# Kernel tuning notes

Hardware: AMD Instinct MI355X
Metric: run time of the kernel (lower is better)

Reference implementation:

```python
import jax, jax.numpy as jnp
import numpy as np
from jax import lax

PH = PW = 7  # patch size


def _unfold2d(x, ph, pw):
    # x: [B, C, H, W] -> patches [B*Ho*Wo, C*ph*pw], channel-major like F.unfold
    B, C, H, W = x.shape
    patches = lax.conv_general_dilated_patches(
        x, filter_shape=(ph, pw), window_strides=(1, 1), padding='VALID')
    # patches: [B, C*ph*pw, Ho, Wo] with feature order (c, i, j) matching F.unfold
    Ho, Wo = H - ph + 1, W - pw + 1
    D = C * ph * pw
    q2d = patches.reshape(B, D, Ho * Wo).transpose(0, 2, 1).reshape(B * Ho * Wo, D)
    return q2d, (B, C, H, W, Ho, Wo, D)


def _fold2d_mean(res, shape_info):
    # res: [B*Ho*Wo, D] patch values -> overlap-add mean image [B, C, H, W]
    B, C, H, W, Ho, Wo, D = shape_info
    res = res.reshape(B, Ho, Wo, C, PH, PW)
    out = jnp.zeros((B, C, H, W), dtype=res.dtype)
    cnt = jnp.zeros((H, W), dtype=res.dtype)
    for di in range(PH):          # small fixed 7x7 loop over patch offsets
        for dj in range(PW):
            out = out.at[:, :, di:di + Ho, dj:dj + Wo].add(
                res[:, :, :, :, di, dj].transpose(0, 3, 1, 2))
            cnt = cnt.at[di:di + Ho, dj:dj + Wo].add(1.0)
    return out / cnt  # reduce='mean'


def setup_inputs() -> dict:
    key = jax.random.key(0)
    k1, k2, k3 = jax.random.split(key, 3)
    query = jax.random.normal(k1, (1, 3, 96, 96), dtype=jnp.float32)
    kmat = jax.random.normal(k2, (8100, 147), dtype=jnp.float32)
    vmat = jax.random.normal(k3, (8100, 147), dtype=jnp.float32)
    return {"query": query, "key": kmat, "value": vmat}


def reference(query, key, value):
    # 1) unfold query image into patch rows [Nq, D]
    q2d, shape_info = _unfold2d(query, PH, PW)
    # 2) nearest-neighbor lookup: squared-euclidean argmin over key rows
    qn = jnp.sum(q2d * q2d, axis=1, keepdims=True)        # [Nq, 1]
    kn = jnp.sum(key * key, axis=1)                       # [Nk]
    dist = qn + kn[None, :] - 2.0 * (q2d @ key.T)         # [Nq, Nk]
    idx = jnp.argmin(dist, axis=1)                        # [Nq]
    # 3) gather matched value patches and fold back (overlap-add mean)
    res = value[idx]                                      # [Nq, D]
    return _fold2d_mean(res, shape_info)
```

## Files before the change

### kernel.cpp

```cpp
#include <hip/hip_runtime.h>


#define NQ 8100
#define NK 8100
#define DD 147
#define HO 90
#define IMG 96
#define NCH 5
#define CST 262144
#define ARRN (NCH * CST)

typedef _Float16 half8 __attribute__((ext_vector_type(8)));
typedef float f32x4 __attribute__((ext_vector_type(4)));

__global__ void k_prep(const float* __restrict__ query, const float* __restrict__ key,
                       _Float16* __restrict__ Qh, _Float16* __restrict__ Ql,
                       _Float16* __restrict__ Kh, _Float16* __restrict__ Kl,
                       float* __restrict__ kn, unsigned long long* __restrict__ fidx64) {
    const int bx = blockIdx.x;
    const bool isK = (blockIdx.y != 0);

    if (bx >= 640) {
        if (!isK) return;
        int wave = threadIdx.x >> 6, lane = threadIdx.x & 63;
        int kb = ((bx - 640) * 4 + wave) * 16;
        for (int r = 0; r < 16; ++r) {
            int k = kb + r;
            float s = 0.f;
            if (k < NK)
                for (int d = lane; d < DD; d += 64) {
                    float v = key[k * DD + d];
                    s += v * v;
                }
#pragma unroll
            for (int off = 32; off; off >>= 1) s += __shfl_down(s, off, 64);
            if (lane == 0) {
                kn[k] = (k < NK) ? s : 1e30f;
                fidx64[k] = 0xFFFFFFFFFFFFFFFFull;
            }
        }
        return;
    }

    int t = bx * 256 + threadIdx.x;
    int c = t >> 15;
    int rem = t & 32767;
    int col = ((rem >> 6) << 4) + (rem & 15);
    int quad = (rem >> 4) & 3;
    int kbase = c * 32 + quad * 8;

    float v[8];
#pragma unroll
    for (int j = 0; j < 8; ++j) {
        int k = kbase + j;
        float x = 0.f;
        if (k < DD && col < NQ) {
            if (isK) {
                x = key[col * DD + k];
            } else {
                int c3 = k / 49, r2 = k - 49 * c3;
                int rr = r2 / 7, ss = r2 - 7 * rr;
                int y = col / HO, xx = col - HO * y;
                x = query[(c3 * IMG + y + rr) * IMG + xx + ss];
            }
        }
        v[j] = x;
    }
    half8 h8, l8;
#pragma unroll
    for (int j = 0; j < 8; ++j) {
        _Float16 h = (_Float16)v[j];
        h8[j] = h;
        l8[j] = (_Float16)((v[j] - (float)h) * 2048.0f);
    }
    if (isK) {
        *(half8*)(Kh + t * 8) = h8;
        *(half8*)(Kl + t * 8) = l8;
    } else {
        *(half8*)(Qh + t * 8) = h8;
        *(half8*)(Ql + t * 8) = l8;
    }
}

__launch_bounds__(256, 2)
__global__ void k_nn(const _Float16* __restrict__ Qh, const _Float16* __restrict__ Ql,
                     const _Float16* __restrict__ Kh, const _Float16* __restrict__ Kl,
                     const float* __restrict__ kn, unsigned long long* __restrict__ out) {
    __shared__ __align__(16) char smem[33792];

    const int tid = (int)threadIdx.x;
    const int wave = tid >> 6, lane = tid & 63;
    const int l15 = lane & 15, quad = lane >> 4;

    const int b = (int)blockIdx.x;
    const int xcd = b & 7;
    const int i = b >> 3;
    const int qt = (xcd >> 1) * 16 + (i & 15);
    const int kt = (xcd & 1) * 32 + (i >> 4);

    const int mbase = (wave >> 1) * 64;
    const int nbase = (wave & 1) * 64;
    const int q0 = qt * 128, n0 = kt * 128;

    const int agrp = (mbase >> 4);
    const int bgrp = (nbase >> 4);
    const _Float16* gQh = Qh + (qt * 8 + agrp) * 512 + lane * 8;
    const _Float16* gQl = Ql + (qt * 8 + agrp) * 512 + lane * 8;
    const _Float16* gKh = Kh + (kt * 8 + bgrp) * 512 + lane * 8;
    const _Float16* gKl = Kl + (kt * 8 + bgrp) * 512 + lane * 8;

    f32x4 acc0[4][4], acc1[4][4];
#pragma unroll
    for (int ii = 0; ii < 4; ++ii)
#pragma unroll
        for (int j = 0; j < 4; ++j) {
            acc0[ii][j] = (f32x4)0.f;
            acc1[ii][j] = (f32x4)0.f;
        }

#pragma unroll
    for (int c = 0; c < NCH; ++c) {
        half8 ah[4], al[4], bh[4], bl[4];
#pragma unroll
        for (int mt = 0; mt < 4; ++mt) {
            ah[mt] = *(const half8*)(gQh + c * CST + mt * 512);
            al[mt] = *(const half8*)(gQl + c * CST + mt * 512);
        }
#pragma unroll
        for (int nt = 0; nt < 4; ++nt) {
            bh[nt] = *(const half8*)(gKh + c * CST + nt * 512);
            bl[nt] = *(const half8*)(gKl + c * CST + nt * 512);
        }

        __builtin_amdgcn_s_setprio(1);
#pragma unroll
        for (int nt = 0; nt < 4; ++nt) {
#pragma unroll
            for (int mt = 0; mt < 4; ++mt) {
                acc0[mt][nt] = __builtin_amdgcn_mfma_f32_16x16x32_f16(ah[mt], bh[nt], acc0[mt][nt], 0, 0, 0);
                acc1[mt][nt] = __builtin_amdgcn_mfma_f32_16x16x32_f16(ah[mt], bl[nt], acc1[mt][nt], 0, 0, 0);
                acc1[mt][nt] = __builtin_amdgcn_mfma_f32_16x16x32_f16(al[mt], bh[nt], acc1[mt][nt], 0, 0, 0);
            }
        }
        __builtin_amdgcn_s_setprio(0);
    }

    float knv[4];
    int nglob[4];
#pragma unroll
    for (int nt = 0; nt < 4; ++nt) {
        nglob[nt] = n0 + nbase + nt * 16 + l15;
        knv[nt] = kn[nglob[nt]];
    }
    unsigned long long* redu = (unsigned long long*)smem;

#pragma unroll
    for (int mt = 0; mt < 4; ++mt)
#pragma unroll
        for (int r = 0; r < 4; ++r) {
            float bv = 1e38f;
            int bn = 0x7fffffff;
#pragma unroll
            for (int nt = 0; nt < 4; ++nt) {
                float d = knv[nt] - 2.0f * (acc0[mt][nt][r] + acc1[mt][nt][r] * (1.0f / 2048.0f));
                if (d < bv) { bv = d; bn = nglob[nt]; }
            }
            int m = mbase + mt * 16 + quad * 4 + r;
            int cidx = (nbase >> 2) + l15;
            unsigned u = __float_as_uint(bv);
            u = (u & 0x80000000u) ? ~u : (u | 0x80000000u);
            redu[m * 33 + cidx] = ((unsigned long long)u << 32) | (unsigned)bn;
        }
    __syncthreads();

    {
        int row = tid >> 1;
        int base = (tid & 1) * 16;
        unsigned long long best = 0xFFFFFFFFFFFFFFFFull;
        const unsigned long long* rp = redu + row * 33 + base;
#pragma unroll
        for (int t2 = 0; t2 < 16; ++t2) {
            unsigned long long v = rp[t2];
            best = (v < best) ? v : best;
        }
        unsigned long long other = __shfl_xor(best, 1, 64);
        best = (other < best) ? other : best;
        if (!(tid & 1)) atomicMin(&out[q0 + row], best);
    }
}

__global__ void k_fold(const float* __restrict__ value,
                       const unsigned long long* __restrict__ fidx64,
                       float* __restrict__ out) {
    int t = blockIdx.x * 256 + threadIdx.x;
    int pix = t >> 3, s = t & 7;
    if (pix >= 3 * IMG * IMG) return;
    int c = pix / (IMG * IMG);
    int rem = pix % (IMG * IMG);
    int Y = rem / IMG, X = rem % IMG;

    float partial = 0.f;
    int yy = Y - s;
    if (s < 7 && (unsigned)yy < (unsigned)HO) {
        const unsigned* fidx32 = (const unsigned*)fidx64;
        const float* vbase = value + c * 49 + s * 7;
        int rows[7];
        bool oks[7];
#pragma unroll
        for (int j = 0; j < 7; ++j) {
            int xx = X - j;
            bool ok = (unsigned)xx < (unsigned)HO;
            int p = ok ? (yy * HO + xx) : 0;
            rows[j] = (int)fidx32[2 * p];
            oks[j] = ok;
        }
#pragma unroll
        for (int j = 0; j < 7; ++j) {
            float v = vbase[rows[j] * DD + j];
            if (oks[j]) partial += v;
        }
    }
    partial += __shfl_down(partial, 4, 8);
    partial += __shfl_down(partial, 2, 8);
    partial += __shfl_down(partial, 1, 8);
    if (s == 0) {
        int i0 = max(0, Y - (HO - 1)), i1 = min(6, Y);
        int j0 = max(0, X - (HO - 1)), j1 = min(6, X);
        float cnt = (float)((i1 - i0 + 1) * (j1 - j0 + 1));
        out[pix] = partial / cnt;
    }
}

extern "C" void kernel_launch(void* const* d_in, const int* in_sizes, int n_in,
                              void* d_out, int out_size, void* d_ws, size_t ws_size,
                              hipStream_t stream) {
    const float* query = (const float*)d_in[0];
    const float* key   = (const float*)d_in[1];
    const float* value = (const float*)d_in[2];
    float* out = (float*)d_out;

    _Float16* Qh = (_Float16*)d_ws;
    _Float16* Ql = Qh + ARRN;
    _Float16* Kh = Ql + ARRN;
    _Float16* Kl = Kh + ARRN;
    float* kn = (float*)(Kl + ARRN);
    unsigned long long* fidx64 = (unsigned long long*)(kn + 8192);

    dim3 gp(768, 2);
    k_prep<<<gp, 256, 0, stream>>>(query, key, Qh, Ql, Kh, Kl, kn, fidx64);
    k_nn<<<4096, 256, 0, stream>>>(Qh, Ql, Kh, Kl, kn, fidx64);
    k_fold<<<864, 256, 0, stream>>>(value, fidx64, out);
}
```

Baseline: 144.2 us.

## Merge split-fp16 accumulators and double-buffer chunk fragment loads in NN kernel

The low half of each split-fp16 value is now stored unscaled, so all three MFMA products go into one accumulator instead of two. This halves accumulator registers and removes the rescale in the epilogue. Fragment loads for the next K chunk are also issued before the current chunk's MFMAs to hide global-load latency. The risk is that unscaled low residuals can underflow into fp16 subnormals, losing precision and possibly changing argmin ties; the register saving is partly spent on the doubled fragment buffers.

Result: no change. 145.3 us (+0.7%).

```diff
diff --git a/kernel.cpp b/kernel.cpp
--- a/kernel.cpp
+++ b/kernel.cpp
@@ -71,7 +71,7 @@
     for (int j = 0; j < 8; ++j) {
         _Float16 h = (_Float16)v[j];
         h8[j] = h;
-        l8[j] = (_Float16)((v[j] - (float)h) * 2048.0f);
+        l8[j] = (_Float16)(v[j] - (float)h);
     }
     if (isK) {
         *(half8*)(Kh + t * 8) = h8;
@@ -109,37 +109,49 @@
     const _Float16* gKh = Kh + (kt * 8 + bgrp) * 512 + lane * 8;
     const _Float16* gKl = Kl + (kt * 8 + bgrp) * 512 + lane * 8;
 
-    f32x4 acc0[4][4], acc1[4][4];
+    f32x4 acc[4][4];
 #pragma unroll
     for (int ii = 0; ii < 4; ++ii)
 #pragma unroll
-        for (int j = 0; j < 4; ++j) {
-            acc0[ii][j] = (f32x4)0.f;
-            acc1[ii][j] = (f32x4)0.f;
-        }
+        for (int j = 0; j < 4; ++j)
+            acc[ii][j] = (f32x4)0.f;
+
+    half8 ah[2][4], al[2][4], bh[2][4], bl[2][4];
+#pragma unroll
+    for (int mt = 0; mt < 4; ++mt) {
+        ah[0][mt] = *(const half8*)(gQh + mt * 512);
+        al[0][mt] = *(const half8*)(gQl + mt * 512);
+    }
+#pragma unroll
+    for (int nt = 0; nt < 4; ++nt) {
+        bh[0][nt] = *(const half8*)(gKh + nt * 512);
+        bl[0][nt] = *(const half8*)(gKl + nt * 512);
+    }
 
 #pragma unroll
     for (int c = 0; c < NCH; ++c) {
-        half8 ah[4], al[4], bh[4], bl[4];
-#pragma unroll
-        for (int mt = 0; mt < 4; ++mt) {
-            ah[mt] = *(const half8*)(gQh + c * CST + mt * 512);
-            al[mt] = *(const half8*)(gQl + c * CST + mt * 512);
-        }
+        const int cur = c & 1, nxt = cur ^ 1;
+        if (c + 1 < NCH) {
+#pragma unroll
+            for (int mt = 0; mt < 4; ++mt) {
+                ah[nxt][mt] = *(const half8*)(gQh + (c + 1) * CST + mt * 512);
+                al[nxt][mt] = *(const half8*)(gQl + (c + 1) * CST + mt * 512);
+            }
+#pragma unroll
+            for (int nt = 0; nt < 4; ++nt) {
+                bh[nxt][nt] = *(const half8*)(gKh + (c + 1) * CST + nt * 512);
+                bl[nxt][nt] = *(const half8*)(gKl + (c + 1) * CST + nt * 512);
+            }
+        }
+
+        __builtin_amdgcn_s_setprio(1);
 #pragma unroll
         for (int nt = 0; nt < 4; ++nt) {
-            bh[nt] = *(const half8*)(gKh + c * CST + nt * 512);
-            bl[nt] = *(const half8*)(gKl + c * CST + nt * 512);
-        }
-
-        __builtin_amdgcn_s_setprio(1);
-#pragma unroll
-        for (int nt = 0; nt < 4; ++nt) {
 #pragma unroll
             for (int mt = 0; mt < 4; ++mt) {
-                acc0[mt][nt] = __builtin_amdgcn_mfma_f32_16x16x32_f16(ah[mt], bh[nt], acc0[mt][nt], 0, 0, 0);
-                acc1[mt][nt] = __builtin_amdgcn_mfma_f32_16x16x32_f16(ah[mt], bl[nt], acc1[mt][nt], 0, 0, 0);
-                acc1[mt][nt] = __builtin_amdgcn_mfma_f32_16x16x32_f16(al[mt], bh[nt], acc1[mt][nt], 0, 0, 0);
+                acc[mt][nt] = __builtin_amdgcn_mfma_f32_16x16x32_f16(ah[cur][mt], bh[cur][nt], acc[mt][nt], 0, 0, 0);
+                acc[mt][nt] = __builtin_amdgcn_mfma_f32_16x16x32_f16(ah[cur][mt], bl[cur][nt], acc[mt][nt], 0, 0, 0);
+                acc[mt][nt] = __builtin_amdgcn_mfma_f32_16x16x32_f16(al[cur][mt], bh[cur][nt], acc[mt][nt], 0, 0, 0);
             }
         }
         __builtin_amdgcn_s_setprio(0);
@@ -162,7 +174,7 @@
             int bn = 0x7fffffff;
 #pragma unroll
             for (int nt = 0; nt < 4; ++nt) {
-                float d = knv[nt] - 2.0f * (acc0[mt][nt][r] + acc1[mt][nt][r] * (1.0f / 2048.0f));
+                float d = knv[nt] - 2.0f * acc[mt][nt][r];
                 if (d < bv) { bv = d; bn = nglob[nt]; }
             }
             int m = mbase + mt * 16 + quad * 4 + r;
```
